# Optimization experiments

Measured on AMD Instinct MI355X. Metric: run time of the kernel, lower is better.

The kernel has to match this reference:

```python
import jax, jax.numpy as jnp
import numpy as np
from jax import lax

D_MODEL = 1024
N_HEADS = 8
D_HEAD = 64
D_INNER = N_HEADS * D_HEAD  # 512
B, T = 4, 4096
LN_EPS = 1e-5
NORM_EPS = 1e-12  # F.normalize default eps


def setup_inputs() -> dict:
    key = jax.random.key(0)
    ks = jax.random.split(key, 6)
    s_proj = (2.0 / (D_MODEL + D_INNER)) ** 0.5  # xavier_uniform-ish std
    x = jax.random.normal(ks[0], (B, T, D_MODEL), jnp.float32)
    Wq = jax.random.normal(ks[1], (D_MODEL, D_INNER), jnp.float32) * s_proj
    Wk = jax.random.normal(ks[2], (D_MODEL, D_INNER), jnp.float32) * s_proj
    Wv = jax.random.normal(ks[3], (D_MODEL, D_INNER), jnp.float32) * s_proj
    Wa = jax.random.normal(ks[4], (D_MODEL, D_INNER), jnp.float32) * s_proj
    ba = jnp.full((D_INNER,), 3.0, jnp.float32)  # nn.init.constant_(W_alpha.bias, 3.0)
    Wo = jax.random.normal(ks[5], (D_INNER, D_MODEL), jnp.float32) * s_proj
    gamma = jnp.ones((D_MODEL,), jnp.float32)
    beta = jnp.zeros((D_MODEL,), jnp.float32)
    return {"x": x, "Wq": Wq, "Wk": Wk, "Wv": Wv, "Wa": Wa, "ba": ba,
            "Wo": Wo, "gamma": gamma, "beta": beta}


def reference(x, Wq, Wk, Wv, Wa, ba, Wo, gamma, beta):
    Bx, Tx, _ = x.shape
    residual = x
    # LayerNorm
    mu = jnp.mean(x, axis=-1, keepdims=True)
    var = jnp.var(x, axis=-1, keepdims=True)
    xn = (x - mu) / jnp.sqrt(var + LN_EPS) * gamma + beta
    # Projections -> (B, T, H, d) -> time-major (T, B, H, d) for scan
    def heads(y):
        return jnp.moveaxis(y.reshape(Bx, Tx, N_HEADS, D_HEAD), 1, 0)
    q = heads(xn @ Wq)
    k = heads(xn @ Wk)
    v = heads(xn @ Wv)
    alpha = jax.nn.sigmoid(heads(xn @ Wa + ba))
    # F.normalize(k, dim=-1)
    knorm = jnp.linalg.norm(k, axis=-1, keepdims=True)
    k = k / jnp.maximum(knorm, NORM_EPS)

    # Recurrence: S_t = diag(a_t) S_{t-1} + k_t v_t^T ; o_t = S_t^T q_t
    def step(S, inp):
        q_t, k_t, v_t, a_t = inp  # each (B, H, d)
        S = a_t[..., None] * S + k_t[..., None] * v_t[..., None, :]  # (B,H,dk,dv)
        o_t = jnp.einsum('bhji,bhj->bhi', S, q_t)
        return S, o_t

    S0 = jnp.zeros((Bx, N_HEADS, D_HEAD, D_HEAD), x.dtype)
    _, outs = lax.scan(step, S0, (q, k, v, alpha))  # outs: (T, B, H, d)
    out = jnp.moveaxis(outs, 0, 1).reshape(Bx, Tx, D_INNER) @ Wo
    return out + residual
```

## Files before the change

kernel.cpp:

```cpp
#include <hip/hip_runtime.h>
#include <stdint.h>

#define NTOK   16384
#define DM     1024
#define DI     512
#define NH     8
#define DH     64
#define CHUNK  64
#define NCH    64
#define NBHC   2048

using short8 = __attribute__((ext_vector_type(8))) short;
using f32x4  = __attribute__((ext_vector_type(4))) float;

__device__ __forceinline__ unsigned short f2bf(float f) {
  union { float f; unsigned int u; } x; x.f = f;
  unsigned int u = x.u;
  return (unsigned short)((u + 0x7fffu + ((u >> 16) & 1u)) >> 16);
}
__device__ __forceinline__ float bf2f(unsigned short h) {
  union { unsigned int u; float f; } x; x.u = ((unsigned int)h) << 16; return x.f;
}

typedef const __attribute__((address_space(1))) void* gp1_t;
typedef __attribute__((address_space(3))) void* lp3_t;
__device__ __forceinline__ void gload_lds16(const void* g, void* l) {
  __builtin_amdgcn_global_load_lds((gp1_t)g, (lp3_t)l, 16, 0, 0);
}

__global__ __launch_bounds__(256) void init_kernel(const float* __restrict__ x,
                                                   const float* __restrict__ gamma,
                                                   const float* __restrict__ beta,
                                                   const float* __restrict__ Wq,
                                                   const float* __restrict__ Wk,
                                                   const float* __restrict__ Wv,
                                                   const float* __restrict__ Wa,
                                                   const float* __restrict__ Wo,
                                                   unsigned short* __restrict__ xn,
                                                   unsigned short* __restrict__ Wt,
                                                   unsigned short* __restrict__ Wot) {
  const int blk = blockIdx.x, tid = threadIdx.x;
  __shared__ float tile[32][33];
  __shared__ float rs_[4], rss_[4];
  if (blk < NTOK) {
    const int row = blk;
    float4 v = ((const float4*)(x + (long)row * DM))[tid];
    float s  = v.x + v.y + v.z + v.w;
    float ss = v.x * v.x + v.y * v.y + v.z * v.z + v.w * v.w;
    #pragma unroll
    for (int off = 32; off > 0; off >>= 1) { s += __shfl_down(s, off); ss += __shfl_down(ss, off); }
    int wave = tid >> 6, lane = tid & 63;
    if (lane == 0) { rs_[wave] = s; rss_[wave] = ss; }
    __syncthreads();
    s  = rs_[0] + rs_[1] + rs_[2] + rs_[3];
    ss = rss_[0] + rss_[1] + rss_[2] + rss_[3];
    float mu   = s * (1.f / DM);
    float var  = ss * (1.f / DM) - mu * mu;
    float rstd = rsqrtf(var + 1e-5f);
    int idx = tid * 4;
    float xv[4] = {v.x, v.y, v.z, v.w};
    unsigned short o[4];
    #pragma unroll
    for (int j = 0; j < 4; ++j) o[j] = f2bf((xv[j] - mu) * rstd * gamma[idx + j] + beta[idx + j]);
    uint2 pk; pk.x = (unsigned)o[0] | ((unsigned)o[1] << 16); pk.y = (unsigned)o[2] | ((unsigned)o[3] << 16);
    *(uint2*)(xn + (long)row * DM + idx) = pk;
  } else if (blk < NTOK + 2048) {
    const int id = blk - NTOK;
    const int z = id >> 9, r9 = id & 511;
    const float* in = (z == 0) ? Wq : (z == 1) ? Wk : (z == 2) ? Wv : Wa;
    unsigned short* o = Wt + (size_t)z * 512 * 1024;
    int bx = (r9 & 15) * 32, by = (r9 >> 4) * 32;
    int tx = tid & 31, ty = tid >> 5;
    #pragma unroll
    for (int r = ty; r < 32; r += 8) tile[r][tx] = in[(long)(by + r) * 512 + bx + tx];
    __syncthreads();
    #pragma unroll
    for (int r = ty; r < 32; r += 8) o[(long)(bx + r) * 1024 + by + tx] = f2bf(tile[tx][r]);
  } else {
    const int id = blk - NTOK - 2048;
    int bx = (id & 31) * 32, by = (id >> 5) * 32;
    int tx = tid & 31, ty = tid >> 5;
    #pragma unroll
    for (int r = ty; r < 32; r += 8) tile[r][tx] = Wo[(long)(by + r) * 1024 + bx + tx];
    __syncthreads();
    #pragma unroll
    for (int r = ty; r < 32; r += 8) Wot[(long)(bx + r) * 512 + by + tx] = f2bf(tile[tx][r]);
  }
}

#define EPSW 264
#define G4_TILE(T_, DOSTAGE_, WAITC_)                                         \
  {                                                                           \
    if (DOSTAGE_) {                                                           \
      const int s_ = (T_) + 3;                                                \
      unsigned short* sb_ = &sm[(s_ & 3) * 16384];                            \
      const long ko_ = (long)s_ * 32;                                         \
      gload_lds16(a0p + ko_, sb_ + dst);                                      \
      gload_lds16(a1p + ko_, sb_ + 4096 + dst);                               \
      gload_lds16(b0p + ko_, sb_ + 8192 + dst);                               \
      gload_lds16(b1p + ko_, sb_ + 12288 + dst);                              \
    }                                                                         \
    const unsigned short* cb_ = &sm[((T_) & 3) * 16384];                      \
    short8 av_[8], bv_[4];                                                    \
    _Pragma("unroll")                                                         \
    for (int mt = 0; mt < 8; ++mt) av_[mt] = *(const short8*)&cb_[aoff + mt * 512]; \
    _Pragma("unroll")                                                         \
    for (int nt = 0; nt < 4; ++nt) bv_[nt] = *(const short8*)&cb_[boff + nt * 512]; \
    __builtin_amdgcn_s_setprio(1);                                            \
    _Pragma("unroll")                                                         \
    for (int mt = 0; mt < 8; ++mt)                                            \
      _Pragma("unroll")                                                       \
      for (int nt = 0; nt < 4; ++nt)                                          \
        acc[mt][nt] = __builtin_amdgcn_mfma_f32_16x16x32_bf16(av_[mt], bv_[nt], acc[mt][nt], 0, 0, 0); \
    __builtin_amdgcn_s_setprio(0);                                            \
    asm volatile("s_waitcnt " WAITC_ ::: "memory");                           \
    __builtin_amdgcn_s_barrier();                                             \
    __builtin_amdgcn_sched_barrier(0);                                        \
  }

__global__ __launch_bounds__(512, 2) void gemm1k(const unsigned short* __restrict__ A,
                                                 const unsigned short* __restrict__ Bt,
                                                 unsigned short* __restrict__ Cb,
                                                 int M, int N, int K) {
  __shared__ __align__(16) unsigned short sm[65536];
  const int tid = threadIdx.x;
  const int wave = tid >> 6, lane = tid & 63;
  const int quad = lane >> 4, l16 = lane & 15;
  const int wm = wave >> 2, wn = wave & 3;

  const int nwg = gridDim.x;
  const int cpx = nwg >> 3;
  const int bid = blockIdx.x;
  const int swz = (bid & 7) * cpx + (bid >> 3);
  const int m0 = (swz & 63) * 256;
  const int n0 = (swz >> 6) * 256;

  const int r2 = tid >> 2;
  const int scol = ((tid & 3) * 8) ^ (((tid >> 3) & 3) * 8);
  const unsigned short* a0p = A + (long)(m0 + r2) * K + scol;
  const unsigned short* a1p = A + (long)(m0 + 128 + r2) * K + scol;
  const unsigned short* b0p = Bt + (long)(n0 + r2) * K + scol;
  const unsigned short* b1p = Bt + (long)(n0 + 128 + r2) * K + scol;
  const int dst = tid * 8;

  const int swzr = (quad * 8) ^ (((l16 >> 1) & 3) * 8);
  const int aoff = (wm * 128 + l16) * 32 + swzr;
  const int boff = 8192 + (wn * 64 + l16) * 32 + swzr;

  f32x4 acc[8][4];
  #pragma unroll
  for (int i = 0; i < 8; ++i)
    #pragma unroll
    for (int j = 0; j < 4; ++j) acc[i][j] = (f32x4){0.f, 0.f, 0.f, 0.f};

  const int NT = K >> 5;

  #pragma unroll
  for (int s = 0; s < 3; ++s) {
    unsigned short* sb = &sm[s * 16384];
    const long ko = (long)s * 32;
    gload_lds16(a0p + ko, sb + dst);
    gload_lds16(a1p + ko, sb + 4096 + dst);
    gload_lds16(b0p + ko, sb + 8192 + dst);
    gload_lds16(b1p + ko, sb + 12288 + dst);
  }
  asm volatile("s_waitcnt vmcnt(8)" ::: "memory");
  __builtin_amdgcn_s_barrier();
  __builtin_amdgcn_sched_barrier(0);

  int t = 0;
  for (; t < NT - 3; ++t) G4_TILE(t, true, "vmcnt(8)");
  G4_TILE(t, false, "vmcnt(4)"); ++t;
  G4_TILE(t, false, "vmcnt(0)"); ++t;
  G4_TILE(t, false, "vmcnt(0)");

  unsigned short* epi = sm;
  #pragma unroll
  for (int h = 0; h < 2; ++h) {
    if (wm == h) {
      #pragma unroll
      for (int fm = 0; fm < 8; ++fm)
        #pragma unroll
        for (int fn = 0; fn < 4; ++fn)
          #pragma unroll
          for (int r = 0; r < 4; ++r)
            epi[(fm * 16 + quad * 4 + r) * EPSW + wn * 64 + fn * 16 + l16] = f2bf(acc[fm][fn][r]);
    }
    __syncthreads();
    #pragma unroll
    for (int i = tid; i < 4096; i += 512) {
      int row = i >> 5, cc = (i & 31) * 8;
      uint4 v = *(const uint4*)&epi[row * EPSW + cc];
      *(uint4*)&Cb[(long)(m0 + h * 128 + row) * N + n0 + cc] = v;
    }
    __syncthreads();
  }
}

__global__ __launch_bounds__(256, 2) void gemm2k(const unsigned short* __restrict__ A,
                                                 const unsigned short* __restrict__ Bt,
                                                 float* __restrict__ Cf,
                                                 const float* __restrict__ resid,
                                                 int M, int N, int K) {
  __shared__ __align__(16) unsigned short sm[32768];
  const int tid = threadIdx.x;
  const int wave = tid >> 6, lane = tid & 63;
  const int quad = lane >> 4, l16 = lane & 15;
  const int wm = wave >> 1, wn = wave & 1;

  const int nwg = gridDim.x;
  const int cpx = nwg >> 3;
  const int bid = blockIdx.x;
  const int swz = (bid & 7) * cpx + (bid >> 3);
  const int m0 = (swz & 127) * 128;
  const int n0 = (swz >> 7) * 128;

  const int r2 = tid >> 2;
  const int scol = ((tid & 3) * 8) ^ (((tid >> 3) & 3) * 8);
  const unsigned short* a0p = A + (long)(m0 + r2) * K + scol;
  const unsigned short* a1p = A + (long)(m0 + 64 + r2) * K + scol;
  const unsigned short* b0p = Bt + (long)(n0 + r2) * K + scol;
  const unsigned short* b1p = Bt + (long)(n0 + 64 + r2) * K + scol;
  const int dst = tid * 8;

  const int swzr = (quad * 8) ^ (((l16 >> 1) & 3) * 8);
  const int aoff = wm * 2048 + l16 * 32 + swzr;
  const int boff = 4096 + wn * 2048 + l16 * 32 + swzr;

  f32x4 acc[4][4];
  #pragma unroll
  for (int i = 0; i < 4; ++i)
    #pragma unroll
    for (int j = 0; j < 4; ++j) acc[i][j] = (f32x4){0.f, 0.f, 0.f, 0.f};

  const int NT = K >> 5;

  #pragma unroll
  for (int s = 0; s < 3; ++s) {
    unsigned short* sb = &sm[s * 8192];
    const long ko = (long)s * 32;
    gload_lds16(a0p + ko, sb + dst);
    gload_lds16(a1p + ko, sb + 2048 + dst);
    gload_lds16(b0p + ko, sb + 4096 + dst);
    gload_lds16(b1p + ko, sb + 6144 + dst);
  }
  asm volatile("s_waitcnt vmcnt(8)" ::: "memory");
  __builtin_amdgcn_s_barrier();
  __builtin_amdgcn_sched_barrier(0);

#define G2_TILE(T_, DOSTAGE_, WAITC_)                                         \
  {                                                                           \
    if (DOSTAGE_) {                                                           \
      const int s_ = (T_) + 3;                                                \
      unsigned short* sb_ = &sm[(s_ & 3) * 8192];                             \
      const long ko_ = (long)s_ * 32;                                         \
      gload_lds16(a0p + ko_, sb_ + dst);                                      \
      gload_lds16(a1p + ko_, sb_ + 2048 + dst);                               \
      gload_lds16(b0p + ko_, sb_ + 4096 + dst);                               \
      gload_lds16(b1p + ko_, sb_ + 6144 + dst);                               \
    }                                                                         \
    const unsigned short* cb_ = &sm[((T_) & 3) * 8192];                       \
    short8 av_[4], bv_[4];                                                    \
    _Pragma("unroll")                                                         \
    for (int mt = 0; mt < 4; ++mt) av_[mt] = *(const short8*)&cb_[aoff + mt * 512]; \
    _Pragma("unroll")                                                         \
    for (int nt = 0; nt < 4; ++nt) bv_[nt] = *(const short8*)&cb_[boff + nt * 512]; \
    __builtin_amdgcn_s_setprio(1);                                            \
    _Pragma("unroll")                                                         \
    for (int mt = 0; mt < 4; ++mt)                                            \
      _Pragma("unroll")                                                       \
      for (int nt = 0; nt < 4; ++nt)                                          \
        acc[mt][nt] = __builtin_amdgcn_mfma_f32_16x16x32_bf16(av_[mt], bv_[nt], acc[mt][nt], 0, 0, 0); \
    __builtin_amdgcn_s_setprio(0);                                            \
    asm volatile("s_waitcnt " WAITC_ ::: "memory");                           \
    __builtin_amdgcn_s_barrier();                                             \
    __builtin_amdgcn_sched_barrier(0);                                        \
  }

  int t = 0;
  for (; t < NT - 3; ++t) G2_TILE(t, true, "vmcnt(8)");
  G2_TILE(t, false, "vmcnt(4)"); ++t;
  G2_TILE(t, false, "vmcnt(0)"); ++t;
  G2_TILE(t, false, "vmcnt(0)");

  unsigned short* epi = sm;
  #pragma unroll
  for (int mt = 0; mt < 4; ++mt)
    #pragma unroll
    for (int nt = 0; nt < 4; ++nt)
      #pragma unroll
      for (int r = 0; r < 4; ++r)
        epi[(wm * 64 + mt * 16 + quad * 4 + r) * 136 + wn * 64 + nt * 16 + l16] = f2bf(acc[mt][nt][r]);
  __syncthreads();
  #pragma unroll
  for (int i = tid; i < 4096; i += 256) {
    int row = i >> 5, cc = (i & 31) * 4;
    long g = (long)(m0 + row) * N + n0 + cc;
    float4 rv = *(const float4*)&resid[g];
    uint2 pv = *(const uint2*)&epi[row * 136 + cc];
    float4 ov;
    ov.x = bf2f((unsigned short)(pv.x & 0xffffu)) + rv.x;
    ov.y = bf2f((unsigned short)(pv.x >> 16))     + rv.y;
    ov.z = bf2f((unsigned short)(pv.y & 0xffffu)) + rv.z;
    ov.w = bf2f((unsigned short)(pv.y >> 16))     + rv.w;
    *(float4*)&Cf[g] = ov;
  }
}

#define TS 72
__global__ __launch_bounds__(256) void prep_intra_kernel(const unsigned short* __restrict__ Cb,
                                                         const float* __restrict__ ba,
                                                         unsigned short* __restrict__ qt,
                                                         float* __restrict__ Dvec,
                                                         unsigned short* __restrict__ Ointra,
                                                         unsigned short* __restrict__ Tt) {
  const int bhc = blockIdx.x;
  const int c = bhc & 63, bh = bhc >> 6;
  const int h = bh & 7, b = bh >> 3;
  const int tid = threadIdx.x;
  __shared__ __align__(16) unsigned short Qb[4096], Kb[4096], Vb[4096], lamB[4096];
  __shared__ __align__(16) unsigned short Vt[64 * TS], Kt[64 * TS];
  __shared__ float rnF[64], lendF[64];
  const long rowbase = ((long)(b * 4096 + c * 64)) * 2048;
  const int hoff = h * 64;

  if (tid < 64) rnF[tid] = 0.f;
  __syncthreads();

  #pragma unroll
  for (int chunk = 0; chunk < 2; ++chunk) {
    int u = chunk * 256 + tid;
    int t = u >> 3, p = u & 7;
    long g = rowbase + (long)t * 2048 + hoff + p * 8;
    uint4 q4 = *(const uint4*)(Cb + g);
    uint4 k4 = *(const uint4*)(Cb + g + 512);
    uint4 v4 = *(const uint4*)(Cb + g + 1024);
    uint4 a4 = *(const uint4*)(Cb + g + 1536);
    *(uint4*)&Qb[u * 8] = q4;
    *(uint4*)&Kb[u * 8] = k4;
    *(uint4*)&Vb[u * 8] = v4;
    const unsigned short* as_ = (const unsigned short*)&a4;
    unsigned short al[8];
    #pragma unroll
    for (int j = 0; j < 8; ++j) {
      float z = bf2f(as_[j]) + ba[hoff + p * 8 + j];
      al[j] = f2bf(1.f / (1.f + __expf(-z)));
    }
    uint4 pa;
    pa.x = (unsigned)al[0] | ((unsigned)al[1] << 16); pa.y = (unsigned)al[2] | ((unsigned)al[3] << 16);
    pa.z = (unsigned)al[4] | ((unsigned)al[5] << 16); pa.w = (unsigned)al[6] | ((unsigned)al[7] << 16);
    *(uint4*)&lamB[u * 8] = pa;
    const unsigned short* ks = (const unsigned short*)&k4;
    float ssq = 0.f;
    #pragma unroll
    for (int j = 0; j < 8; ++j) { float kv = bf2f(ks[j]); ssq += kv * kv; }
    atomicAdd(&rnF[t], ssq);
  }
  __syncthreads();

  if (tid < 64) {
    int d = tid; float cum = 1.f;
    #pragma unroll
    for (int t = 0; t < 64; ++t) {
      cum *= bf2f(lamB[t * 64 + d]);
      lamB[t * 64 + d] = f2bf(cum);
    }
    Dvec[(long)bhc * 64 + d] = cum;
    lendF[d] = cum;
  } else if (tid < 128) {
    int t = tid - 64;
    rnF[t] = 1.f / fmaxf(sqrtf(rnF[t]), 1e-12f);
  }
  __syncthreads();

  #pragma unroll
  for (int j = 0; j < 16; ++j) {
    int e = j * 256 + tid;
    int t = e >> 6;
    float lam = bf2f(lamB[e]);
    float kn = bf2f(Kb[e]) * rnF[t];
    Qb[e] = f2bf(bf2f(Qb[e]) * lam);
    Kb[e] = f2bf(kn / lam);
  }
  __syncthreads();

  {
    const long obase = (long)bhc * 4096;
    uint4* gq = (uint4*)(qt + obase);
    const uint4* lq = (const uint4*)Qb;
    gq[tid] = lq[tid]; gq[tid + 256] = lq[tid + 256];
  }

  const long base = (long)bhc * 4096;
  const int wave = tid >> 6, lane = tid & 63, quad = lane >> 4, l16 = lane & 15;
  const int mrow = wave * 16 + l16;
  unsigned short* Ps = lamB;

  union { short8 v; short s[8]; } aI;
  aI.v = (short8){0,0,0,0,0,0,0,0};
  {
    int target = ((wave & 1) * 16 + l16) - quad * 8;
    if (target >= 0 && target < 8) aI.s[target] = (short)0x3F80;
  }
  const int bsel = (wave >> 1) * 32;

  {
    short8 a0 = *(const short8*)&Qb[mrow * 64 + quad * 8];
    short8 a1 = *(const short8*)&Qb[mrow * 64 + 32 + quad * 8];
    #pragma unroll
    for (int nt = 0; nt < 4; ++nt) {
      short8 b0 = *(const short8*)&Kb[(nt * 16 + l16) * 64 + quad * 8];
      short8 b1 = *(const short8*)&Kb[(nt * 16 + l16) * 64 + 32 + quad * 8];
      f32x4 acc = (f32x4){0.f, 0.f, 0.f, 0.f};
      acc = __builtin_amdgcn_mfma_f32_16x16x32_bf16(a0, b0, acc, 0, 0, 0);
      acc = __builtin_amdgcn_mfma_f32_16x16x32_bf16(a1, b1, acc, 0, 0, 0);
      #pragma unroll
      for (int r = 0; r < 4; ++r) {
        int t = wave * 16 + quad * 4 + r, u = nt * 16 + l16;
        Ps[t * 64 + u] = (u <= t) ? f2bf(acc[r]) : (unsigned short)0;
      }
    }
  }
  #pragma unroll
  for (int nt = 0; nt < 4; ++nt) {
    short8 bv = *(const short8*)&Vb[(nt * 16 + l16) * 64 + bsel + quad * 8];
    short8 bk = *(const short8*)&Kb[(nt * 16 + l16) * 64 + bsel + quad * 8];
    f32x4 av = (f32x4){0.f, 0.f, 0.f, 0.f};
    f32x4 ak = (f32x4){0.f, 0.f, 0.f, 0.f};
    av = __builtin_amdgcn_mfma_f32_16x16x32_bf16(aI.v, bv, av, 0, 0, 0);
    ak = __builtin_amdgcn_mfma_f32_16x16x32_bf16(aI.v, bk, ak, 0, 0, 0);
    #pragma unroll
    for (int r = 0; r < 4; ++r) {
      int i = wave * 16 + quad * 4 + r, t = nt * 16 + l16;
      Vt[i * TS + t] = f2bf(av[r]);
      Kt[i * TS + t] = f2bf(ak[r]);
    }
  }
  __syncthreads();

  {
    short8 a0 = *(const short8*)&Ps[mrow * 64 + quad * 8];
    short8 a1 = *(const short8*)&Ps[mrow * 64 + 32 + quad * 8];
    #pragma unroll
    for (int nt = 0; nt < 4; ++nt) {
      short8 b0 = *(const short8*)&Vt[(nt * 16 + l16) * TS + quad * 8];
      short8 b1 = *(const short8*)&Vt[(nt * 16 + l16) * TS + 32 + quad * 8];
      f32x4 acc = (f32x4){0.f, 0.f, 0.f, 0.f};
      acc = __builtin_amdgcn_mfma_f32_16x16x32_bf16(a0, b0, acc, 0, 0, 0);
      acc = __builtin_amdgcn_mfma_f32_16x16x32_bf16(a1, b1, acc, 0, 0, 0);
      #pragma unroll
      for (int r = 0; r < 4; ++r) {
        int t = wave * 16 + quad * 4 + r, i = nt * 16 + l16;
        Vb[t * 64 + i] = f2bf(acc[r]);
      }
    }
  }
  {
    short8 a0 = *(const short8*)&Vt[mrow * TS + quad * 8];
    short8 a1 = *(const short8*)&Vt[mrow * TS + 32 + quad * 8];
    #pragma unroll
    for (int nt = 0; nt < 4; ++nt) {
      short8 b0 = *(const short8*)&Kt[(nt * 16 + l16) * TS + quad * 8];
      short8 b1 = *(const short8*)&Kt[(nt * 16 + l16) * TS + 32 + quad * 8];
      f32x4 acc = (f32x4){0.f, 0.f, 0.f, 0.f};
      acc = __builtin_amdgcn_mfma_f32_16x16x32_bf16(a0, b0, acc, 0, 0, 0);
      acc = __builtin_amdgcn_mfma_f32_16x16x32_bf16(a1, b1, acc, 0, 0, 0);
      float le = lendF[nt * 16 + l16];
      #pragma unroll
      for (int r = 0; r < 4; ++r) {
        int i = wave * 16 + quad * 4 + r, j = nt * 16 + l16;
        Kb[i * 64 + j] = f2bf(acc[r] * le);
      }
    }
  }
  __syncthreads();
  {
    const uint4* ov = (const uint4*)Vb; uint4* og = (uint4*)(Ointra + base);
    const uint4* tv = (const uint4*)Kb; uint4* tg = (uint4*)(Tt + base);
    og[tid] = ov[tid]; og[tid + 256] = ov[tid + 256];
    tg[tid] = tv[tid]; tg[tid + 256] = tv[tid + 256];
  }
}

__global__ __launch_bounds__(256) void scan_kernel(const unsigned short* __restrict__ Tt,
                                                   const float* __restrict__ Dvec,
                                                   unsigned short* __restrict__ Sst) {
  const int bh = blockIdx.x;
  const int e = blockIdx.y * 256 + threadIdx.x;
  const int j = e & 63;
  float S = 0.f;
  for (int c = 0; c < 64; ++c) {
    const long idx = ((long)(bh * 64 + c)) * 4096 + e;
    const float dj = Dvec[((long)(bh * 64 + c)) * 64 + j];
    Sst[idx] = f2bf(S);
    S = dj * S + bf2f(Tt[idx]);
  }
}

__global__ __launch_bounds__(256) void combine_kernel(const unsigned short* __restrict__ qt,
                                                      const unsigned short* __restrict__ Sst,
                                                      const unsigned short* __restrict__ Ointra,
                                                      unsigned short* __restrict__ O) {
  const int bhc = blockIdx.x;
  const int c = bhc & 63, bh = bhc >> 6;
  const int h = bh & 7, b = bh >> 3;
  const long base = (long)bhc * 4096;
  __shared__ __align__(16) unsigned short Qs[4096], Sb[4096], Os[4096];
  const int tid = threadIdx.x;
  {
    const uint4* gq = (const uint4*)(qt + base);     uint4* lq = (uint4*)Qs;
    const uint4* gs = (const uint4*)(Sst + base);    uint4* ls = (uint4*)Sb;
    const uint4* go = (const uint4*)(Ointra + base); uint4* lo = (uint4*)Os;
    lq[tid] = gq[tid]; lq[tid + 256] = gq[tid + 256];
    ls[tid] = gs[tid]; ls[tid + 256] = gs[tid + 256];
    lo[tid] = go[tid]; lo[tid + 256] = go[tid + 256];
  }
  __syncthreads();
  const int wave = tid >> 6, lane = tid & 63, quad = lane >> 4, l16 = lane & 15;
  const int mrow = wave * 16 + l16;
  short8 a0 = *(const short8*)&Qs[mrow * 64 + quad * 8];
  short8 a1 = *(const short8*)&Qs[mrow * 64 + 32 + quad * 8];
  #pragma unroll
  for (int nt = 0; nt < 4; ++nt) {
    f32x4 acc;
    #pragma unroll
    for (int r = 0; r < 4; ++r) {
      int t = wave * 16 + quad * 4 + r, i = nt * 16 + l16;
      acc[r] = bf2f(Os[t * 64 + i]);
    }
    short8 b0 = *(const short8*)&Sb[(nt * 16 + l16) * 64 + quad * 8];
    short8 b1 = *(const short8*)&Sb[(nt * 16 + l16) * 64 + 32 + quad * 8];
    acc = __builtin_amdgcn_mfma_f32_16x16x32_bf16(a0, b0, acc, 0, 0, 0);
    acc = __builtin_amdgcn_mfma_f32_16x16x32_bf16(a1, b1, acc, 0, 0, 0);
    #pragma unroll
    for (int r = 0; r < 4; ++r) {
      int t = wave * 16 + quad * 4 + r, i = nt * 16 + l16;
      O[((long)(b * 4096 + c * 64 + t)) * 512 + h * 64 + i] = f2bf(acc[r]);
    }
  }
}

extern "C" void kernel_launch(void* const* d_in, const int* in_sizes, int n_in,
                              void* d_out, int out_size, void* d_ws, size_t ws_size,
                              hipStream_t stream) {
  const float* x     = (const float*)d_in[0];
  const float* Wq    = (const float*)d_in[1];
  const float* Wk    = (const float*)d_in[2];
  const float* Wv    = (const float*)d_in[3];
  const float* Wa    = (const float*)d_in[4];
  const float* ba    = (const float*)d_in[5];
  const float* Wo    = (const float*)d_in[6];
  const float* gamma = (const float*)d_in[7];
  const float* beta  = (const float*)d_in[8];
  float* out = (float*)d_out;

  char* ws = (char*)d_ws;
  const size_t KB = 1024;
  unsigned short* Wt     = (unsigned short*)(ws + 0 * KB);
  unsigned short* Wot    = (unsigned short*)(ws + 4096 * KB);
  float*          Dvec   = (float*)         (ws + 5120 * KB);
  unsigned short* qt     = (unsigned short*)(ws + 5632 * KB);
  unsigned short* Ttb    = (unsigned short*)(ws + 22016 * KB);
  unsigned short* Sst    = (unsigned short*)(ws + 38400 * KB);
  unsigned short* xn     = (unsigned short*)(ws + 54784 * KB);
  unsigned short* Ointra = (unsigned short*)(ws + 54784 * KB);
  unsigned short* Ob     = (unsigned short*)(ws + 71168 * KB);
  unsigned short* Cb     = (unsigned short*)(ws + 87552 * KB);

  init_kernel<<<NTOK + 2048 + 512, 256, 0, stream>>>(x, gamma, beta, Wq, Wk, Wv, Wa, Wo, xn, Wt, Wot);
  gemm1k<<<512, 512, 0, stream>>>(xn, Wt, Cb, NTOK, 2048, 1024);
  prep_intra_kernel<<<NBHC, 256, 0, stream>>>(Cb, ba, qt, Dvec, Ointra, Ttb);
  scan_kernel<<<dim3(32, 16), 256, 0, stream>>>(Ttb, Dvec, Sst);
  combine_kernel<<<NBHC, 256, 0, stream>>>(qt, Sst, Ointra, Ob);
  gemm2k<<<1024, 256, 0, stream>>>(Ob, Wot, out, x, NTOK, 1024, 512);
}
```

Before: 312.4 us.

## Split gemm1 into two launches, parallelize chunk cumprod, prefetch scan loads

The first projection GEMM is now two launches of 256 workgroups, each covering half of the M rows through a row offset, in place of one launch of 512. In prep_intra, the serial 64-step cumulative product of the decay factors, done by 64 threads, becomes a four-segment parallel prefix using all 256 threads, with segment products combined through shared memory. The scan kernel now uses precomputed base pointers and software-prefetches the next chunk's T and decay values to hide load latency in the serial recurrence. Splitting the GEMM adds one extra launch and may cut per-launch occupancy.

```diff
diff --git a/kernel.cpp b/kernel.cpp
--- a/kernel.cpp
+++ b/kernel.cpp
@@ -121,19 +121,18 @@
 __global__ __launch_bounds__(512, 2) void gemm1k(const unsigned short* __restrict__ A,
                                                  const unsigned short* __restrict__ Bt,
                                                  unsigned short* __restrict__ Cb,
-                                                 int M, int N, int K) {
+                                                 int N, int K, int moff) {
   __shared__ __align__(16) unsigned short sm[65536];
   const int tid = threadIdx.x;
   const int wave = tid >> 6, lane = tid & 63;
   const int quad = lane >> 4, l16 = lane & 15;
   const int wm = wave >> 2, wn = wave & 3;
 
-  const int nwg = gridDim.x;
-  const int cpx = nwg >> 3;
+  const int cpx = gridDim.x >> 3;
   const int bid = blockIdx.x;
   const int swz = (bid & 7) * cpx + (bid >> 3);
-  const int m0 = (swz & 63) * 256;
-  const int n0 = (swz >> 6) * 256;
+  const int m0 = ((swz & 31) << 8) + moff;
+  const int n0 = (swz >> 5) << 8;
 
   const int r2 = tid >> 2;
   const int scol = ((tid & 3) * 8) ^ (((tid >> 3) & 3) * 8);
@@ -253,7 +252,7 @@
     if (DOSTAGE_) {                                                           \
       const int s_ = (T_) + 3;                                                \
       unsigned short* sb_ = &sm[(s_ & 3) * 8192];                             \
-      const long ko_ = (long)s_ * 32;                                         \
+      const long ko_ = (long)s_ * 32;                                        \
       gload_lds16(a0p + ko_, sb_ + dst);                                      \
       gload_lds16(a1p + ko_, sb_ + 2048 + dst);                               \
       gload_lds16(b0p + ko_, sb_ + 4096 + dst);                               \
@@ -321,6 +320,7 @@
   __shared__ __align__(16) unsigned short Qb[4096], Kb[4096], Vb[4096], lamB[4096];
   __shared__ __align__(16) unsigned short Vt[64 * TS], Kt[64 * TS];
   __shared__ float rnF[64], lendF[64];
+  __shared__ float segP[256];
   const long rowbase = ((long)(b * 4096 + c * 64)) * 2048;
   const int hoff = h * 64;
 
@@ -358,19 +358,19 @@
   }
   __syncthreads();
 
-  if (tid < 64) {
-    int d = tid; float cum = 1.f;
-    #pragma unroll
-    for (int t = 0; t < 64; ++t) {
-      cum *= bf2f(lamB[t * 64 + d]);
-      lamB[t * 64 + d] = f2bf(cum);
-    }
-    Dvec[(long)bhc * 64 + d] = cum;
-    lendF[d] = cum;
-  } else if (tid < 128) {
-    int t = tid - 64;
-    rnF[t] = 1.f / fmaxf(sqrtf(rnF[t]), 1e-12f);
-  }
+  if (tid < 64) rnF[tid] = 1.f / fmaxf(sqrtf(rnF[tid]), 1e-12f);
+  const int dd = tid & 63, seg = tid >> 6;
+  float cseg[16]; float run = 1.f;
+  #pragma unroll
+  for (int i = 0; i < 16; ++i) { run *= bf2f(lamB[(seg * 16 + i) * 64 + dd]); cseg[i] = run; }
+  segP[tid] = run;
+  __syncthreads();
+  float pre = 1.f;
+  #pragma unroll
+  for (int s = 0; s < 3; ++s) { float v = segP[s * 64 + dd]; pre = (s < seg) ? pre * v : pre; }
+  #pragma unroll
+  for (int i = 0; i < 16; ++i) lamB[(seg * 16 + i) * 64 + dd] = f2bf(pre * cseg[i]);
+  if (seg == 3) { float cum = pre * run; Dvec[(long)bhc * 64 + dd] = cum; lendF[dd] = cum; }
   __syncthreads();
 
   #pragma unroll
@@ -488,13 +488,20 @@
   const int bh = blockIdx.x;
   const int e = blockIdx.y * 256 + threadIdx.x;
   const int j = e & 63;
+  const unsigned short* tp = Tt + (long)bh * 262144 + e;
+  const float* dp = Dvec + (long)bh * 4096 + j;
+  unsigned short* sp = Sst + (long)bh * 262144 + e;
   float S = 0.f;
-  for (int c = 0; c < 64; ++c) {
-    const long idx = ((long)(bh * 64 + c)) * 4096 + e;
-    const float dj = Dvec[((long)(bh * 64 + c)) * 64 + j];
-    Sst[idx] = f2bf(S);
-    S = dj * S + bf2f(Tt[idx]);
-  }
+  float tv = bf2f(tp[0]);
+  float dj = dp[0];
+  for (int c = 0; c < 63; ++c) {
+    float tv_n = bf2f(tp[(c + 1) * 4096]);
+    float dj_n = dp[(c + 1) * 64];
+    sp[(long)c * 4096] = f2bf(S);
+    S = dj * S + tv;
+    tv = tv_n; dj = dj_n;
+  }
+  sp[63L * 4096] = f2bf(S);
 }
 
 __global__ __launch_bounds__(256) void combine_kernel(const unsigned short* __restrict__ qt,
@@ -568,7 +575,8 @@
   unsigned short* Cb     = (unsigned short*)(ws + 87552 * KB);
 
   init_kernel<<<NTOK + 2048 + 512, 256, 0, stream>>>(x, gamma, beta, Wq, Wk, Wv, Wa, Wo, xn, Wt, Wot);
-  gemm1k<<<512, 512, 0, stream>>>(xn, Wt, Cb, NTOK, 2048, 1024);
+  gemm1k<<<256, 512, 0, stream>>>(xn, Wt, Cb, 2048, 1024, 0);
+  gemm1k<<<256, 512, 0, stream>>>(xn, Wt, Cb, 2048, 1024, 8192);
   prep_intra_kernel<<<NBHC, 256, 0, stream>>>(Cb, ba, qt, Dvec, Ointra, Ttb);
   scan_kernel<<<dim3(32, 16), 256, 0, stream>>>(Ttb, Dvec, Sst);
   combine_kernel<<<NBHC, 256, 0, stream>>>(qt, Sst, Ointra, Ob);
```

New measurement: 323.4 us. +3.5%, slower.
